# Kernel tuning notes

Measured on AMD Instinct MI355X. Metric: run time of the kernel, lower is better.

Reference implementation:

```python
import jax, jax.numpy as jnp
import numpy as np

B, C, N = 16, 64, 2048
K, KS, OC = 20, 20, 64
BN_EPS = 1e-5


def setup_inputs() -> dict:
    key = jax.random.key(0)
    k1, k2, k3, k4 = jax.random.split(key, 4)
    feature = jax.random.normal(k1, (B, C, N), dtype=jnp.float32)
    neigh_indexs = jax.random.randint(k2, (B * N, K), 0, B * N, dtype=jnp.int64)
    permatrix = jax.random.normal(k3, (B * N, K, KS), dtype=jnp.float32)
    conv_w = jax.random.normal(k4, (OC, 2 * C), dtype=jnp.float32) * 0.05  # 1x1 conv weight
    conv_b = jnp.zeros((OC,), dtype=jnp.float32)
    gamma = jnp.ones((OC,), dtype=jnp.float32)
    beta = jnp.zeros((OC,), dtype=jnp.float32)
    return {"feature": feature, "neigh_indexs": neigh_indexs, "permatrix": permatrix,
            "conv_w": conv_w, "conv_b": conv_b, "gamma": gamma, "beta": beta}


def _forward(feature, neigh_indexs, permatrix, conv_w, conv_b, gamma, beta):
    bsize, num_feat, num_pts = feature.shape
    # [B, C, N] -> [B*N, C]
    flat = jnp.transpose(feature, (0, 2, 1)).reshape(bsize * num_pts, num_feat)
    # neighbor gather: [B*N, K, C] -> [B*N, C, K]
    feats = jnp.transpose(flat[neigh_indexs], (0, 2, 1))
    f_repeat = jnp.broadcast_to(feats[:, :, 0:1], feats.shape)
    f_relative = feats - f_repeat
    feats = jnp.concatenate([f_repeat, f_relative], axis=1)  # [B*N, 2C, K]
    # per-point small matmul with permutation matrix: [B*N, 2C, KS]
    feats = jnp.einsum('nck,nks->ncs', feats, permatrix)
    # 1x1 conv over channel dim: [B*N, OC, KS]
    out = jnp.einsum('ncs,oc->nos', feats, conv_w) + conv_b[None, :, None]
    # max over neighbors, reshape to [B, OC, N]
    out = jnp.max(out, axis=-1).reshape(bsize, num_pts, -1)
    out = jnp.transpose(out, (0, 2, 1))  # [B, OC, N]
    # BatchNorm1d (training-mode forward: biased var over batch & points)
    mean = jnp.mean(out, axis=(0, 2), keepdims=True)
    var = jnp.var(out, axis=(0, 2), keepdims=True)
    out = (out - mean) * jax.lax.rsqrt(var + BN_EPS)
    return out * gamma[None, :, None] + beta[None, :, None]


def reference(feature, neigh_indexs, permatrix, conv_w, conv_b, gamma, beta):
    return _forward(feature, neigh_indexs, permatrix, conv_w, conv_b, gamma, beta)
```

## Files before the change

kernel.cpp:

```cpp
#include <hip/hip_runtime.h>

#define B_   16
#define C_   64
#define N_   2048
#define M_   (B_ * N_)
#define K_   20
#define KS_  20
#define OC_  64
#define NW2  8192

__global__ __launch_bounds__(256) void k_project(
    const float* __restrict__ feat,
    const float* __restrict__ conv_w,
    float* __restrict__ pq)
{
    const int lane = threadIdx.x & 63;
    const int wg   = blockIdx.x * 4 + (threadIdx.x >> 6);
    float w2[64], wd[64];
    const float4* cw4 = (const float4*)conv_w;
    #pragma unroll
    for (int j = 0; j < 16; ++j) {
        float4 a = cw4[lane * 32 + j];
        float4 b = cw4[lane * 32 + 16 + j];
        w2[4*j+0] = b.x; w2[4*j+1] = b.y; w2[4*j+2] = b.z; w2[4*j+3] = b.w;
        wd[4*j+0] = a.x - b.x; wd[4*j+1] = a.y - b.y;
        wd[4*j+2] = a.z - b.z; wd[4*j+3] = a.w - b.w;
    }
    const int m0 = wg * 8;
    int b0 = m0 >> 11, p0 = m0 & 2047;
    float fv = feat[((size_t)(b0 * 64 + lane)) * 2048 + p0];
    for (int mi = 0; mi < 8; ++mi) {
        const int m = m0 + mi;
        float fnext = 0.f;
        if (mi < 7) {
            const int mn = m + 1;
            fnext = feat[((size_t)((mn >> 11) * 64 + lane)) * 2048 + (mn & 2047)];
        }
        float p0a = 0.f, p1a = 0.f, q0a = 0.f, q1a = 0.f;
        #pragma unroll
        for (int c = 0; c < 32; ++c) {
            float f0 = __int_as_float(
                __builtin_amdgcn_readlane(__float_as_int(fv), c));
            float f1 = __int_as_float(
                __builtin_amdgcn_readlane(__float_as_int(fv), c + 32));
            p0a = fmaf(w2[c], f0, p0a);
            p1a = fmaf(w2[c + 32], f1, p1a);
            q0a = fmaf(wd[c], f0, q0a);
            q1a = fmaf(wd[c + 32], f1, q1a);
        }
        pq[(size_t)m * 128 + lane]      = p0a + p1a;
        pq[(size_t)m * 128 + 64 + lane] = q0a + q1a;
        fv = fnext;
    }
}

__global__ __launch_bounds__(256) void k_points(
    const float* __restrict__ pq,
    const int*   __restrict__ nidx,
    const float* __restrict__ perm,
    const float* __restrict__ conv_b,
    float* __restrict__ pre,
    float* __restrict__ partials)
{
    __shared__ __align__(16) float plds[4 * 4 * 404];
    const int tid  = threadIdx.x;
    const int lane = tid & 63;
    const int og   = lane & 15;
    const int p    = lane >> 4;
    const int wv   = tid >> 6;
    const int wg   = (int)blockIdx.x * 4 + wv;
    const int nb   = wg * 4;
    const int n    = nb + p;
    float* wbuf = &plds[wv * 1616];

    int2 iv2 = make_int2(0, 0);
    if (lane < 40) iv2 = ((const int2*)(nidx + (size_t)nb * 20))[lane];

    #pragma unroll
    for (int pp = 0; pp < 4; ++pp) {
        const float4* src = (const float4*)(perm + (size_t)(nb + pp) * 400);
        float* dst = wbuf + pp * 404;
        float4 v0 = src[lane];
        *(float4*)(dst + lane * 4) = v0;
        if (lane < 36) {
            float4 v1 = src[64 + lane];
            *(float4*)(dst + 256 + lane * 4) = v1;
        }
    }

    const float4 bias = *(const float4*)(conv_b + og * 4);

    int ik0 = __shfl(iv2.x, p * 10);
    const float* pqb = pq + (size_t)ik0 * 128 + og * 4;
    float4 q4  = *(const float4*)(pqb + 64);
    float4 pkc = *(const float4*)(pqb);

    __syncthreads();

    float acc[4][20];
    #pragma unroll
    for (int s = 0; s < 20; ++s) {
        acc[0][s] = bias.x; acc[1][s] = bias.y;
        acc[2][s] = bias.z; acc[3][s] = bias.w;
    }

    const float* gbase = wbuf + p * 404;
    #pragma unroll
    for (int k = 0; k < 20; ++k) {
        float4 pkn = pkc;
        if (k < 19) {
            const int kk = k + 1;
            int src = p * 10 + (kk >> 1);
            int ikn = (kk & 1) ? __shfl(iv2.y, src) : __shfl(iv2.x, src);
            pkn = *(const float4*)(pq + (size_t)ikn * 128 + og * 4);
        }
        float t[4];
        t[0] = pkc.x + q4.x; t[1] = pkc.y + q4.y;
        t[2] = pkc.z + q4.z; t[3] = pkc.w + q4.w;
        #pragma unroll
        for (int c = 0; c < 5; ++c) {
            float4 m4 = *(const float4*)(gbase + k * 20 + c * 4);
            #pragma unroll
            for (int j = 0; j < 4; ++j) {
                acc[j][c*4+0] = fmaf(t[j], m4.x, acc[j][c*4+0]);
                acc[j][c*4+1] = fmaf(t[j], m4.y, acc[j][c*4+1]);
                acc[j][c*4+2] = fmaf(t[j], m4.z, acc[j][c*4+2]);
                acc[j][c*4+3] = fmaf(t[j], m4.w, acc[j][c*4+3]);
            }
        }
        pkc = pkn;
    }

    float mv[4];
    #pragma unroll
    for (int j = 0; j < 4; ++j) {
        float m = acc[j][0];
        #pragma unroll
        for (int s = 1; s < 20; ++s) m = fmaxf(m, acc[j][s]);
        mv[j] = m;
    }
    *(float4*)(pre + (size_t)n * 64 + og * 4) = make_float4(mv[0], mv[1], mv[2], mv[3]);

    float sv[4], sw[4];
    #pragma unroll
    for (int j = 0; j < 4; ++j) {
        float v = mv[j], w = mv[j] * mv[j];
        v += __shfl_xor(v, 16); v += __shfl_xor(v, 32);
        w += __shfl_xor(w, 16); w += __shfl_xor(w, 32);
        sv[j] = v; sw[j] = w;
    }
    if (lane < 16) {
        *(float4*)(partials + (size_t)wg * 128 + lane * 4)
            = make_float4(sv[0], sv[1], sv[2], sv[3]);
        *(float4*)(partials + (size_t)wg * 128 + 64 + lane * 4)
            = make_float4(sw[0], sw[1], sw[2], sw[3]);
    }
}

__global__ __launch_bounds__(256) void k_red1(
    const float* __restrict__ partials,
    float* __restrict__ mid)
{
    const int t = threadIdx.x;
    const int c = t & 127, rh = t >> 7;
    const float* base = partials + (size_t)blockIdx.x * 64 * 128;
    float s = 0.f;
    for (int i = rh; i < 64; i += 2) s += base[(size_t)i * 128 + c];
    __shared__ float sh[256];
    sh[t] = s;
    __syncthreads();
    if (t < 128) mid[(size_t)blockIdx.x * 128 + t] = sh[t] + sh[t + 128];
}

__global__ __launch_bounds__(256) void k_red2(
    const float* __restrict__ mid,
    const float* __restrict__ gamma,
    const float* __restrict__ beta,
    float* __restrict__ stats)
{
    const int t = threadIdx.x;
    const int c = t & 127, rh = t >> 7;
    double s = 0.0;
    for (int i = rh; i < 128; i += 2) s += (double)mid[(size_t)i * 128 + c];
    __shared__ double shd[256];
    __shared__ double tot[128];
    shd[t] = s;
    __syncthreads();
    if (t < 128) tot[t] = shd[t] + shd[t + 128];
    __syncthreads();
    if (t < 64) {
        const double inv_n = 1.0 / (double)M_;
        double mean = tot[t] * inv_n;
        double var  = tot[t + 64] * inv_n - mean * mean;
        double inv  = 1.0 / sqrt(var + 1e-5);
        double sc   = (double)gamma[t] * inv;
        stats[t]      = (float)sc;
        stats[64 + t] = (float)((double)beta[t] - mean * sc);
    }
}

__global__ __launch_bounds__(256) void k_apply(
    const float* __restrict__ pre,
    const float* __restrict__ stats,
    float* __restrict__ out)
{
    __shared__ float tile[64 * 65];
    __shared__ float scl[64];
    __shared__ float shf[64];
    const int tid = threadIdx.x;
    if (tid < 64)       scl[tid]      = stats[tid];
    else if (tid < 128) shf[tid - 64] = stats[tid];
    __syncthreads();
    const int b  = blockIdx.x >> 5;
    const int pt = (blockIdx.x & 31) * 64;
    const int c  = tid & 63;
    const int r0 = tid >> 6;
    #pragma unroll
    for (int i = 0; i < 16; ++i) {
        const int r = i * 4 + r0;
        float v = pre[((size_t)(b * 2048 + pt + r)) * 64 + c];
        tile[c * 65 + r] = fmaf(v, scl[c], shf[c]);
    }
    __syncthreads();
    #pragma unroll
    for (int i = 0; i < 16; ++i) {
        const int o = i * 4 + r0;
        out[((size_t)(b * 64 + o)) * 2048 + pt + c] = tile[o * 65 + c];
    }
}

extern "C" void kernel_launch(void* const* d_in, const int* in_sizes, int n_in,
                              void* d_out, int out_size, void* d_ws, size_t ws_size,
                              hipStream_t stream) {
    const float* feat   = (const float*)d_in[0];
    const int*   nidx   = (const int*)  d_in[1];
    const float* perm   = (const float*)d_in[2];
    const float* conv_w = (const float*)d_in[3];
    const float* conv_b = (const float*)d_in[4];
    const float* gamma  = (const float*)d_in[5];
    const float* beta   = (const float*)d_in[6];
    float* out = (float*)d_out;

    char* ws = (char*)d_ws;
    size_t off = 0;
    float* pq       = (float*)(ws + off); off += (size_t)M_ * 128 * 4;
    float* pre      = (float*)(ws + off); off += (size_t)M_ * 64 * 4;
    float* partials = (float*)(ws + off); off += (size_t)NW2 * 128 * 4;
    float* mid      = pq;
    float* stats    = pq + 128 * 128;

    hipLaunchKernelGGL(k_project, dim3(1024), dim3(256), 0, stream, feat, conv_w, pq);
    hipLaunchKernelGGL(k_points,  dim3(2048), dim3(256), 0, stream, pq, nidx, perm,
                       conv_b, pre, partials);
    hipLaunchKernelGGL(k_red1,    dim3(128),  dim3(256), 0, stream, partials, mid);
    hipLaunchKernelGGL(k_red2,    dim3(1),    dim3(256), 0, stream, mid, gamma,
                       beta, stats);
    hipLaunchKernelGGL(k_apply,   dim3(512),  dim3(256), 0, stream, pre, stats, out);
}
```

Baseline: 185.4 us.

## Make k_points persistent and prefetch next tile's permatrix and indices into registers

```diff
diff --git a/kernel.cpp b/kernel.cpp
--- a/kernel.cpp
+++ b/kernel.cpp
@@ -8,6 +8,7 @@
 #define KS_  20
 #define OC_  64
 #define NW2  8192
+#define NWAVES 3072
 
 __global__ __launch_bounds__(256) void k_project(
     const float* __restrict__ feat,
@@ -68,92 +69,122 @@
     const int og   = lane & 15;
     const int p    = lane >> 4;
     const int wv   = tid >> 6;
-    const int wg   = (int)blockIdx.x * 4 + wv;
-    const int nb   = wg * 4;
-    const int n    = nb + p;
     float* wbuf = &plds[wv * 1616];
-
-    int2 iv2 = make_int2(0, 0);
-    if (lane < 40) iv2 = ((const int2*)(nidx + (size_t)nb * 20))[lane];
-
-    #pragma unroll
-    for (int pp = 0; pp < 4; ++pp) {
-        const float4* src = (const float4*)(perm + (size_t)(nb + pp) * 400);
-        float* dst = wbuf + pp * 404;
-        float4 v0 = src[lane];
-        *(float4*)(dst + lane * 4) = v0;
-        if (lane < 36) {
-            float4 v1 = src[64 + lane];
-            *(float4*)(dst + 256 + lane * 4) = v1;
-        }
-    }
+    const float* gbase = wbuf + p * 404;
 
     const float4 bias = *(const float4*)(conv_b + og * 4);
 
-    int ik0 = __shfl(iv2.x, p * 10);
-    const float* pqb = pq + (size_t)ik0 * 128 + og * 4;
-    float4 q4  = *(const float4*)(pqb + 64);
-    float4 pkc = *(const float4*)(pqb);
-
-    __syncthreads();
-
-    float acc[4][20];
-    #pragma unroll
-    for (int s = 0; s < 20; ++s) {
-        acc[0][s] = bias.x; acc[1][s] = bias.y;
-        acc[2][s] = bias.z; acc[3][s] = bias.w;
-    }
-
-    const float* gbase = wbuf + p * 404;
-    #pragma unroll
-    for (int k = 0; k < 20; ++k) {
-        float4 pkn = pkc;
-        if (k < 19) {
-            const int kk = k + 1;
-            int src = p * 10 + (kk >> 1);
-            int ikn = (kk & 1) ? __shfl(iv2.y, src) : __shfl(iv2.x, src);
-            pkn = *(const float4*)(pq + (size_t)ikn * 128 + og * 4);
-        }
-        float t[4];
-        t[0] = pkc.x + q4.x; t[1] = pkc.y + q4.y;
-        t[2] = pkc.z + q4.z; t[3] = pkc.w + q4.w;
-        #pragma unroll
-        for (int c = 0; c < 5; ++c) {
-            float4 m4 = *(const float4*)(gbase + k * 20 + c * 4);
+    int wg = (int)blockIdx.x * 4 + wv;
+
+    float4 st[8];
+    int4 iv4 = make_int4(0, 0, 0, 0);
+    {
+        const int nb = wg * 4;
+        if (lane < 20) iv4 = ((const int4*)(nidx + (size_t)nb * 20))[lane];
+        #pragma unroll
+        for (int pp = 0; pp < 4; ++pp) {
+            const float4* src = (const float4*)(perm + (size_t)(nb + pp) * 400);
+            st[pp] = src[lane];
+            if (lane < 36) st[4 + pp] = src[64 + lane];
+        }
+    }
+
+    while (wg < NW2) {
+        const int nb = wg * 4;
+        const int n  = nb + p;
+        const int nwg = (wg + NWAVES < NW2) ? (wg + NWAVES) : 0;
+
+        #pragma unroll
+        for (int pp = 0; pp < 4; ++pp) {
+            float* dst = wbuf + pp * 404;
+            *(float4*)(dst + lane * 4) = st[pp];
+            if (lane < 36) *(float4*)(dst + 256 + lane * 4) = st[4 + pp];
+        }
+
+        int4 ivn = make_int4(0, 0, 0, 0);
+        {
+            const int nbn = nwg * 4;
+            if (lane < 20) ivn = ((const int4*)(nidx + (size_t)nbn * 20))[lane];
             #pragma unroll
-            for (int j = 0; j < 4; ++j) {
-                acc[j][c*4+0] = fmaf(t[j], m4.x, acc[j][c*4+0]);
-                acc[j][c*4+1] = fmaf(t[j], m4.y, acc[j][c*4+1]);
-                acc[j][c*4+2] = fmaf(t[j], m4.z, acc[j][c*4+2]);
-                acc[j][c*4+3] = fmaf(t[j], m4.w, acc[j][c*4+3]);
+            for (int pp = 0; pp < 4; ++pp) {
+                const float4* src = (const float4*)(perm + (size_t)(nbn + pp) * 400);
+                st[pp] = src[lane];
+                if (lane < 36) st[4 + pp] = src[64 + lane];
             }
         }
-        pkc = pkn;
-    }
-
-    float mv[4];
-    #pragma unroll
-    for (int j = 0; j < 4; ++j) {
-        float m = acc[j][0];
-        #pragma unroll
-        for (int s = 1; s < 20; ++s) m = fmaxf(m, acc[j][s]);
-        mv[j] = m;
-    }
-    *(float4*)(pre + (size_t)n * 64 + og * 4) = make_float4(mv[0], mv[1], mv[2], mv[3]);
-
-    float sv[4], sw[4];
-    #pragma unroll
-    for (int j = 0; j < 4; ++j) {
-        float v = mv[j], w = mv[j] * mv[j];
-        v += __shfl_xor(v, 16); v += __shfl_xor(v, 32);
-        w += __shfl_xor(w, 16); w += __shfl_xor(w, 32);
-        sv[j] = v; sw[j] = w;
-    }
-    if (lane < 16) {
-        *(float4*)(partials + (size_t)wg * 128 + lane * 4)
-            = make_float4(sv[0], sv[1], sv[2], sv[3]);
-        *(float4*)(partials + (size_t)wg * 128 + 64 + lane * 4)
-            = make_float4(sw[0], sw[1], sw[2], sw[3]);
+
+        int ik0 = __shfl(iv4.x, p * 5);
+        const float* pqb = pq + (size_t)ik0 * 128 + og * 4;
+        float4 q4  = *(const float4*)(pqb + 64);
+        float4 pkc = *(const float4*)(pqb);
+
+        float acc[4][20];
+        #pragma unroll
+        for (int s = 0; s < 20; ++s) {
+            acc[0][s] = bias.x; acc[1][s] = bias.y;
+            acc[2][s] = bias.z; acc[3][s] = bias.w;
+        }
+
+        #pragma unroll
+        for (int k = 0; k < 20; ++k) {
+            float4 pkn = pkc;
+            if (k < 19) {
+                const int kk = k + 1;
+                const int sl = p * 5 + (kk >> 2);
+                int ikn;
+                switch (kk & 3) {
+                    case 0: ikn = __shfl(iv4.x, sl); break;
+                    case 1: ikn = __shfl(iv4.y, sl); break;
+                    case 2: ikn = __shfl(iv4.z, sl); break;
+                    default: ikn = __shfl(iv4.w, sl); break;
+                }
+                pkn = *(const float4*)(pq + (size_t)ikn * 128 + og * 4);
+            }
+            float t[4];
+            t[0] = pkc.x + q4.x; t[1] = pkc.y + q4.y;
+            t[2] = pkc.z + q4.z; t[3] = pkc.w + q4.w;
+            #pragma unroll
+            for (int c = 0; c < 5; ++c) {
+                float4 m4 = *(const float4*)(gbase + k * 20 + c * 4);
+                #pragma unroll
+                for (int j = 0; j < 4; ++j) {
+                    acc[j][c*4+0] = fmaf(t[j], m4.x, acc[j][c*4+0]);
+                    acc[j][c*4+1] = fmaf(t[j], m4.y, acc[j][c*4+1]);
+                    acc[j][c*4+2] = fmaf(t[j], m4.z, acc[j][c*4+2]);
+                    acc[j][c*4+3] = fmaf(t[j], m4.w, acc[j][c*4+3]);
+                }
+            }
+            pkc = pkn;
+        }
+
+        float mv[4];
+        #pragma unroll
+        for (int j = 0; j < 4; ++j) {
+            float m = acc[j][0];
+            #pragma unroll
+            for (int s = 1; s < 20; ++s) m = fmaxf(m, acc[j][s]);
+            mv[j] = m;
+        }
+        *(float4*)(pre + (size_t)n * 64 + og * 4)
+            = make_float4(mv[0], mv[1], mv[2], mv[3]);
+
+        float sv[4], sw[4];
+        #pragma unroll
+        for (int j = 0; j < 4; ++j) {
+            float v = mv[j], w = mv[j] * mv[j];
+            v += __shfl_xor(v, 16); v += __shfl_xor(v, 32);
+            w += __shfl_xor(w, 16); w += __shfl_xor(w, 32);
+            sv[j] = v; sw[j] = w;
+        }
+        if (lane < 16) {
+            *(float4*)(partials + (size_t)wg * 128 + lane * 4)
+                = make_float4(sv[0], sv[1], sv[2], sv[3]);
+            *(float4*)(partials + (size_t)wg * 128 + 64 + lane * 4)
+                = make_float4(sw[0], sw[1], sw[2], sw[3]);
+        }
+
+        iv4 = ivn;
+        wg += NWAVES;
     }
 }
 
@@ -250,7 +281,7 @@
     float* stats    = pq + 128 * 128;
 
     hipLaunchKernelGGL(k_project, dim3(1024), dim3(256), 0, stream, feat, conv_w, pq);
-    hipLaunchKernelGGL(k_points,  dim3(2048), dim3(256), 0, stream, pq, nidx, perm,
+    hipLaunchKernelGGL(k_points,  dim3(768),  dim3(256), 0, stream, pq, nidx, perm,
                        conv_b, pre, partials);
     hipLaunchKernelGGL(k_red1,    dim3(128),  dim3(256), 0, stream, partials, mid);
     hipLaunchKernelGGL(k_red2,    dim3(1),    dim3(256), 0, stream, mid, gamma,
```

Result: slower. 213.7 us (+15.2%).
